# Kernel tuning notes

Measured on AMD Instinct MI355X. Metric: run time of the kernel, lower is better.

The kernel has to match this reference:

```python
import jax, jax.numpy as jnp
import numpy as np

N_NODES = 50000
N_EDGES = 800000
N_GRAPHS = 128
HIDDEN = 64
HEADS = 2
OUT = 4
NEG_SLOPE = 0.2
ALPHA_FLAG = 0.05


def _gat_conv(x, src, dst, W, a_src, a_dst, b):
    # PyG GATConv, concat=False (mean over heads), self-loops already appended.
    N = x.shape[0]
    H, C = a_src.shape
    xh = (x @ W).reshape(N, H, C)                       # [N,H,C]
    s_src = (xh * a_src).sum(-1)                        # [N,H]
    s_dst = (xh * a_dst).sum(-1)                        # [N,H]
    e = s_src[src] + s_dst[dst]                         # [E,H]
    e = jnp.where(e > 0, e, NEG_SLOPE * e)              # LeakyReLU(0.2)
    emax = jax.ops.segment_max(e, dst, num_segments=N)  # per-dst softmax max
    emax = jnp.where(jnp.isfinite(emax), emax, 0.0)
    p = jnp.exp(e - emax[dst])
    denom = jax.ops.segment_sum(p, dst, num_segments=N)
    alpha = p / (denom[dst] + 1e-16)                    # [E,H]
    out = jax.ops.segment_sum(alpha[:, :, None] * xh[src], dst, num_segments=N)
    return out.mean(axis=1) + b                         # [N,HIDDEN]


def setup_inputs() -> dict:
    key = jax.random.key(0)
    ks = jax.random.split(key, 32)
    f = lambda k, shape, s=0.1: (jax.random.normal(k, shape) * s).astype(jnp.float32)
    inp = {}
    inp['x_all'] = jax.random.normal(ks[0], (N_NODES, 8), dtype=jnp.float32)
    inp['climber'] = jax.random.normal(ks[1], (N_GRAPHS, 4), dtype=jnp.float32)
    inp['edge_index'] = jax.random.randint(ks[2], (2, N_EDGES), 0, N_NODES)
    inp['batch'] = jnp.sort(jax.random.randint(ks[3], (N_NODES,), 0, N_GRAPHS))
    H = HIDDEN
    inp['W_in'] = f(ks[4], (6, H)); inp['b_in'] = jnp.zeros((H,), jnp.float32)
    inp['W_c'] = f(ks[5], (4, H)); inp['b_c'] = jnp.zeros((H,), jnp.float32)
    inp['W_f1'] = f(ks[6], (H, 2 * H)); inp['b_f1'] = jnp.zeros((2 * H,), jnp.float32)
    inp['W_f2'] = f(ks[7], (H, 2 * H)); inp['b_f2'] = jnp.zeros((2 * H,), jnp.float32)
    inp['W_g1'] = f(ks[8], (H, HEADS * H)); inp['a_src1'] = f(ks[9], (HEADS, H)); inp['a_dst1'] = f(ks[10], (HEADS, H)); inp['b_g1'] = jnp.zeros((H,), jnp.float32)
    inp['W_g2'] = f(ks[11], (H, HEADS * H)); inp['a_src2'] = f(ks[12], (HEADS, H)); inp['a_dst2'] = f(ks[13], (HEADS, H)); inp['b_g2'] = jnp.zeros((H,), jnp.float32)
    inp['W_cl1'] = f(ks[14], (H, H)); inp['b_cl1'] = jnp.zeros((H,), jnp.float32)
    inp['W_cl2'] = f(ks[15], (H, OUT)); inp['b_cl2'] = jnp.zeros((OUT,), jnp.float32)
    inp['W_fh1'] = f(ks[16], (2, 8), 0.001); inp['b_fh1'] = jnp.zeros((8,), jnp.float32)
    inp['W_fh2'] = f(ks[17], (8, OUT), 0.001); inp['b_fh2'] = jnp.zeros((OUT,), jnp.float32)
    return inp


def reference(x_all, climber, edge_index, batch, W_in, b_in, W_c, b_c,
              W_f1, b_f1, W_f2, b_f2,
              W_g1, a_src1, a_dst1, b_g1,
              W_g2, a_src2, a_dst2, b_g2,
              W_cl1, b_cl1, W_cl2, b_cl2,
              W_fh1, b_fh1, W_fh2, b_fh2):
    N = x_all.shape[0]
    flags = x_all[:, -2:]
    x = x_all[:, :-2]
    # climber embedding (eval mode -> dropout is identity)
    c = jax.nn.relu(climber @ W_c + b_c)                 # [G,H]
    x = x @ W_in + b_in                                  # [N,H]
    # FiLM 1
    gb = c @ W_f1 + b_f1
    gamma, beta = jnp.split(gb, 2, axis=-1)
    x = x * (1.0 + gamma[batch]) + beta[batch]
    # add self-loops (PyG GATConv default)
    loop = jnp.arange(N, dtype=edge_index.dtype)
    src = jnp.concatenate([edge_index[0], loop])
    dst = jnp.concatenate([edge_index[1], loop])
    x = jax.nn.relu(_gat_conv(x, src, dst, W_g1, a_src1, a_dst1, b_g1))
    # FiLM 2
    gb = c @ W_f2 + b_f2
    gamma, beta = jnp.split(gb, 2, axis=-1)
    x = x * (1.0 + gamma[batch]) + beta[batch]
    x = jax.nn.relu(_gat_conv(x, src, dst, W_g2, a_src2, a_dst2, b_g2))
    logits_main = jax.nn.relu(x @ W_cl1 + b_cl1) @ W_cl2 + b_cl2
    logits_flag = jax.nn.relu(flags @ W_fh1 + b_fh1) @ W_fh2 + b_fh2
    return logits_main + ALPHA_FLAG * logits_flag
```

## Files before the change

kernel.cpp:

```cpp
#include <hip/hip_runtime.h>
#include <hip/hip_fp16.h>

#define NEG_SLOPE 0.2f
#define ALPHA_FLAG 0.05f

typedef _Float16 h2t __attribute__((ext_vector_type(2)));
union h2u { unsigned u; h2t h; __half2 hh; float f; };
static __device__ __forceinline__ h2t u_as_h2(unsigned u) { h2u c; c.u = u; return c.h; }
static __device__ __forceinline__ float h2_as_f(__half2 h) { h2u c; c.hh = h; return c.f; }
static __device__ __forceinline__ h2t f_as_h2(float f) { h2u c; c.f = f; return c.h; }

static inline size_t align256(size_t x) { return (x + 255) & ~(size_t)255; }

__global__ void prep_kernel(const float* __restrict__ climber,
                            const float* __restrict__ W_c, const float* __restrict__ b_c,
                            const float* __restrict__ W_f1, const float* __restrict__ b_f1,
                            const float* __restrict__ W_f2, const float* __restrict__ b_f2,
                            float* __restrict__ gb1, float* __restrict__ gb2) {
    __shared__ float c_sh[64];
    int g = blockIdx.x, t = threadIdx.x;
    if (t < 64) {
        float acc = b_c[t];
#pragma unroll
        for (int k = 0; k < 4; ++k) acc = fmaf(climber[g * 4 + k], W_c[k * 64 + t], acc);
        c_sh[t] = fmaxf(acc, 0.f);
    }
    __syncthreads();
    float a1 = b_f1[t], a2 = b_f2[t];
#pragma unroll 8
    for (int h = 0; h < 64; ++h) {
        float cv = c_sh[h];
        a1 = fmaf(cv, W_f1[h * 128 + t], a1);
        a2 = fmaf(cv, W_f2[h * 128 + t], a2);
    }
    gb1[g * 128 + t] = a1;
    gb2[g * 128 + t] = a2;
}

__global__ void init_counts_kernel(int* __restrict__ counts, int N) {
    int i = blockIdx.x * blockDim.x + threadIdx.x;
    if (i < N) counts[i] = 1;
}

__global__ void hist_kernel(const int* __restrict__ dst, int E, int* __restrict__ counts) {
    int i = blockIdx.x * blockDim.x + threadIdx.x;
    if (i < E) atomicAdd(&counts[dst[i]], 1);
}

#define SCAN_CHUNK 1024
__global__ void scan_partial_kernel(const int* __restrict__ counts, int* __restrict__ block_sums, int N) {
    __shared__ int sh[256];
    int b = blockIdx.x, t = threadIdx.x;
    int idx0 = b * SCAN_CHUNK + t * 4;
    int s = 0;
    if (idx0 + 3 < N) {
        int4 v = *(const int4*)&counts[idx0];
        s = v.x + v.y + v.z + v.w;
    } else {
#pragma unroll
        for (int u = 0; u < 4; ++u) if (idx0 + u < N) s += counts[idx0 + u];
    }
    sh[t] = s;
    __syncthreads();
#pragma unroll
    for (int off = 128; off; off >>= 1) {
        if (t < off) sh[t] += sh[t + off];
        __syncthreads();
    }
    if (t == 0) block_sums[b] = sh[0];
}

__global__ void scan_blocksums_kernel(const int* __restrict__ block_sums, int* __restrict__ block_bases,
                                      int nb, int* __restrict__ row_ptr, int N) {
    __shared__ int sh[256];
    int t = threadIdx.x;
    int v = (t < nb) ? block_sums[t] : 0;
    sh[t] = v;
    __syncthreads();
#pragma unroll
    for (int off = 1; off < 256; off <<= 1) {
        int add = (t >= off) ? sh[t - off] : 0;
        __syncthreads();
        sh[t] += add;
        __syncthreads();
    }
    if (t < nb) block_bases[t] = sh[t] - v;
    if (t == nb - 1) row_ptr[N] = sh[t];
}

__global__ void scan_final_kernel(const int* __restrict__ counts, const int* __restrict__ block_bases,
                                  int* __restrict__ row_ptr, int* __restrict__ fill, int N) {
    __shared__ int sh[256];
    int b = blockIdx.x, t = threadIdx.x;
    int idx0 = b * SCAN_CHUNK + t * 4;
    int c[4];
    if (idx0 + 3 < N) {
        int4 v = *(const int4*)&counts[idx0];
        c[0] = v.x; c[1] = v.y; c[2] = v.z; c[3] = v.w;
    } else {
#pragma unroll
        for (int u = 0; u < 4; ++u) c[u] = (idx0 + u < N) ? counts[idx0 + u] : 0;
    }
    int s = c[0] + c[1] + c[2] + c[3];
    sh[t] = s;
    __syncthreads();
#pragma unroll
    for (int off = 1; off < 256; off <<= 1) {
        int add = (t >= off) ? sh[t - off] : 0;
        __syncthreads();
        sh[t] += add;
        __syncthreads();
    }
    int run = block_bases[b] + sh[t] - s;
#pragma unroll
    for (int u = 0; u < 4; ++u) {
        if (idx0 + u < N) {
            row_ptr[idx0 + u] = run;
            fill[idx0 + u] = run;
            run += c[u];
        }
    }
}

__global__ void scatter_kernel(const int* __restrict__ src, const int* __restrict__ dst,
                               int E, int N, int* __restrict__ fill, int* __restrict__ csr_src) {
    int i = blockIdx.x * blockDim.x + threadIdx.x;
    if (i >= E + N) return;
    int s, d;
    if (i < E) { s = src[i]; d = dst[i]; }
    else       { s = i - E; d = s; }
    int pos = atomicAdd(&fill[d], 1);
    csr_src[pos] = s;
}

#define XH_NB 32
__global__ __launch_bounds__(256, 4) void xh_kernel(
    const float* __restrict__ x, const float* __restrict__ W_g,
    const float* __restrict__ a_src, const float* __restrict__ a_dst,
    __half* __restrict__ xh, float* __restrict__ s_src, float* __restrict__ s_dst,
    int N, int in_mode,
    const float* __restrict__ x_all, const int* __restrict__ batch,
    const float* __restrict__ W_in, const float* __restrict__ b_in,
    const float* __restrict__ gb1) {
    __shared__ float x_sh[XH_NB * 64];
    __shared__ float win_sh[6 * 64 + 64];
    int t = threadIdx.x;
    int base = blockIdx.x * XH_NB;
    if (in_mode) {
        for (int i = t; i < 448; i += 256)
            win_sh[i] = (i < 384) ? W_in[i] : b_in[i - 384];
        __syncthreads();
        int nd = t >> 3;
        int jb = (t & 7) * 8;
        int n = base + nd;
        if (n < N) {
            float4 a = *(const float4*)&x_all[(size_t)n * 8];
            float2 b = *(const float2*)&x_all[(size_t)n * 8 + 4];
            float xa[6] = {a.x, a.y, a.z, a.w, b.x, b.y};
            int g = batch[n];
            const float* gbrow = &gb1[g * 128];
#pragma unroll
            for (int jj = 0; jj < 8; ++jj) {
                int j = jb + jj;
                float acc = win_sh[384 + j];
#pragma unroll
                for (int k = 0; k < 6; ++k) acc = fmaf(xa[k], win_sh[k * 64 + j], acc);
                x_sh[nd * 64 + j] = acc * (1.f + gbrow[j]) + gbrow[64 + j];
            }
        } else {
#pragma unroll
            for (int jj = 0; jj < 8; ++jj) x_sh[nd * 64 + jb + jj] = 0.f;
        }
    } else {
        int nvalid = N - base; if (nvalid > XH_NB) nvalid = XH_NB;
        int nfloats = nvalid * 64;
#pragma unroll
        for (int rep = 0; rep < 2; ++rep) {
            int i = t * 4 + rep * 1024;
            float4 v = (i < nfloats) ? *(const float4*)&x[(size_t)base * 64 + i]
                                     : make_float4(0.f, 0.f, 0.f, 0.f);
            *(float4*)&x_sh[i] = v;
        }
    }
    __syncthreads();
    int c = t & 63;
    int g = t >> 6;
    float acc0[8], acc1[8];
#pragma unroll
    for (int i = 0; i < 8; ++i) { acc0[i] = 0.f; acc1[i] = 0.f; }
    const float* W0 = W_g + c;
    const float* W1 = W_g + 64 + c;
#pragma unroll 2
    for (int k = 0; k < 64; k += 4) {
        float w0[4], w1[4];
#pragma unroll
        for (int u = 0; u < 4; ++u) { w0[u] = W0[(k + u) * 128]; w1[u] = W1[(k + u) * 128]; }
#pragma unroll
        for (int i = 0; i < 8; ++i) {
            float4 xv = *(const float4*)&x_sh[(g * 8 + i) * 64 + k];
            acc0[i] = fmaf(xv.x, w0[0], acc0[i]);
            acc0[i] = fmaf(xv.y, w0[1], acc0[i]);
            acc0[i] = fmaf(xv.z, w0[2], acc0[i]);
            acc0[i] = fmaf(xv.w, w0[3], acc0[i]);
            acc1[i] = fmaf(xv.x, w1[0], acc1[i]);
            acc1[i] = fmaf(xv.y, w1[1], acc1[i]);
            acc1[i] = fmaf(xv.z, w1[2], acc1[i]);
            acc1[i] = fmaf(xv.w, w1[3], acc1[i]);
        }
    }
    float as0 = a_src[c], ad0 = a_dst[c];
    float as1 = a_src[64 + c], ad1 = a_dst[64 + c];
#pragma unroll
    for (int i = 0; i < 8; ++i) {
        int n = base + g * 8 + i;
        float ps0 = acc0[i] * as0, pd0 = acc0[i] * ad0;
        float ps1 = acc1[i] * as1, pd1 = acc1[i] * ad1;
#pragma unroll
        for (int off = 32; off; off >>= 1) {
            ps0 += __shfl_xor(ps0, off); pd0 += __shfl_xor(pd0, off);
            ps1 += __shfl_xor(ps1, off); pd1 += __shfl_xor(pd1, off);
        }
        if (n < N) {
            if (c == 0) {
                s_src[n * 2 + 0] = ps0; s_src[n * 2 + 1] = ps1;
                s_dst[n * 2 + 0] = pd0; s_dst[n * 2 + 1] = pd1;
            }
            __half2 hv = __floats2half2_rn(acc0[i], acc1[i]);
            *(__half2*)&xh[(size_t)n * 128 + c * 2] = hv;
        }
    }
}

static __device__ __forceinline__ float dot2acc(unsigned xbits, h2t w, float acc) {
#if __has_builtin(__builtin_amdgcn_fdot2)
    return __builtin_amdgcn_fdot2(u_as_h2(xbits), w, acc, false);
#else
    h2u cx; cx.u = xbits;
    float2 xf = __half22float2(cx.hh);
    h2u cw; cw.h = w;
    float2 wf = __half22float2(cw.hh);
    return fmaf(xf.x, wf.x, fmaf(xf.y, wf.y, acc));
#endif
}

__global__ __launch_bounds__(256) void agg_kernel(
    const __half* __restrict__ xh, const float* __restrict__ s_src,
    const float* __restrict__ s_dst, const int* __restrict__ row_ptr,
    const int* __restrict__ csr_src, const float* __restrict__ b_g,
    const int* __restrict__ batch, const float* __restrict__ gb_film,
    float* __restrict__ xout, int N, int mode,
    const float* __restrict__ x_all,
    const float* __restrict__ W_cl1, const float* __restrict__ b_cl1,
    const float* __restrict__ W_cl2, const float* __restrict__ b_cl2,
    const float* __restrict__ W_fh1, const float* __restrict__ b_fh1,
    const float* __restrict__ W_fh2, const float* __restrict__ b_fh2,
    float* __restrict__ out) {
    __shared__ float2 ps_sh[4][64];
    __shared__ float vh_sh[4][64];
    int lane = threadIdx.x & 63;
    int w = threadIdx.x >> 6;
    int n = (blockIdx.x * blockDim.x + threadIdx.x) >> 6;
    if (n >= N) return;
    int beg = row_ptr[n], end = row_ptr[n + 1];
    int deg = end - beg;
    float2 sd = *(const float2*)&s_dst[n * 2];
    const char* xhb = (const char*)xh;
    int sub = lane >> 4;
    unsigned q16 = (unsigned)(lane & 15) * 16u;
    float acc[4] = {0.f, 0.f, 0.f, 0.f};

    if (deg <= 64) {
        float p0 = 0.f, p1 = 0.f; unsigned sb = 0;
        if (lane < deg) {
            int s = csr_src[beg + lane];
            sb = (unsigned)s << 8;
            float2 ss = *(const float2*)&s_src[s * 2];
            float e0 = ss.x + sd.x, e1 = ss.y + sd.y;
            e0 = (e0 > 0.f) ? e0 : NEG_SLOPE * e0;
            e1 = (e1 > 0.f) ? e1 : NEG_SLOPE * e1;
            p0 = __expf(e0); p1 = __expf(e1);
        }
        float dp0 = p0, dp1 = p1;
#pragma unroll
        for (int off = 32; off; off >>= 1) {
            dp0 += __shfl_xor(dp0, off);
            dp1 += __shfl_xor(dp1, off);
        }
        float i0 = 0.5f / (dp0 + 1e-16f), i1 = 0.5f / (dp1 + 1e-16f);
        ps_sh[w][lane] = make_float2(h2_as_f(__floats2half2_rn(p0 * i0, p1 * i1)),
                                     __uint_as_float(sb));
        int mr = (deg + 3) & ~3;
        for (int j = 0; j < mr; j += 4) {
            float2 ps = ps_sh[w][j + sub];
            h2t wpk = f_as_h2(ps.x);
            unsigned voff = __float_as_uint(ps.y) + q16;
            uint4 hv = *(const uint4*)(xhb + voff);
            acc[0] = dot2acc(hv.x, wpk, acc[0]);
            acc[1] = dot2acc(hv.y, wpk, acc[1]);
            acc[2] = dot2acc(hv.z, wpk, acc[2]);
            acc[3] = dot2acc(hv.w, wpk, acc[3]);
        }
    } else {
        float dp0 = 0.f, dp1 = 0.f;
        for (int chunk = beg; chunk < end; chunk += 64) {
            int m = end - chunk; if (m > 64) m = 64;
            if (lane < m) {
                int s = csr_src[chunk + lane];
                float2 ss = *(const float2*)&s_src[s * 2];
                float e0 = ss.x + sd.x, e1 = ss.y + sd.y;
                e0 = (e0 > 0.f) ? e0 : NEG_SLOPE * e0;
                e1 = (e1 > 0.f) ? e1 : NEG_SLOPE * e1;
                dp0 += __expf(e0); dp1 += __expf(e1);
            }
        }
#pragma unroll
        for (int off = 32; off; off >>= 1) {
            dp0 += __shfl_xor(dp0, off);
            dp1 += __shfl_xor(dp1, off);
        }
        float i0 = 0.5f / (dp0 + 1e-16f), i1 = 0.5f / (dp1 + 1e-16f);
        for (int chunk = beg; chunk < end; chunk += 64) {
            int m = end - chunk; if (m > 64) m = 64;
            float p0 = 0.f, p1 = 0.f; unsigned sb = 0;
            if (lane < m) {
                int s = csr_src[chunk + lane];
                sb = (unsigned)s << 8;
                float2 ss = *(const float2*)&s_src[s * 2];
                float e0 = ss.x + sd.x, e1 = ss.y + sd.y;
                e0 = (e0 > 0.f) ? e0 : NEG_SLOPE * e0;
                e1 = (e1 > 0.f) ? e1 : NEG_SLOPE * e1;
                p0 = __expf(e0); p1 = __expf(e1);
            }
            ps_sh[w][lane] = make_float2(h2_as_f(__floats2half2_rn(p0 * i0, p1 * i1)),
                                         __uint_as_float(sb));
            int mr = (m + 3) & ~3;
            for (int j = 0; j < mr; j += 4) {
                float2 ps = ps_sh[w][j + sub];
                h2t wpk = f_as_h2(ps.x);
                unsigned voff = __float_as_uint(ps.y) + q16;
                uint4 hv = *(const uint4*)(xhb + voff);
                acc[0] = dot2acc(hv.x, wpk, acc[0]);
                acc[1] = dot2acc(hv.y, wpk, acc[1]);
                acc[2] = dot2acc(hv.z, wpk, acc[2]);
                acc[3] = dot2acc(hv.w, wpk, acc[3]);
            }
        }
    }
#pragma unroll
    for (int u = 0; u < 4; ++u) {
        acc[u] += __shfl_xor(acc[u], 16);
        acc[u] += __shfl_xor(acc[u], 32);
    }
    if (lane < 16) *(float4*)&vh_sh[w][lane * 4] = make_float4(acc[0], acc[1], acc[2], acc[3]);
    float v = vh_sh[w][lane] + b_g[lane];
    v = fmaxf(v, 0.f);
    if (mode == 0) {
        int g = batch[n];
        v = v * (1.f + gb_film[g * 128 + lane]) + gb_film[g * 128 + 64 + lane];
        xout[(size_t)n * 64 + lane] = v;
        return;
    }
    vh_sh[w][lane] = v;
    float h = b_cl1[lane];
#pragma unroll 4
    for (int k = 0; k < 64; k += 4) {
        float4 vq = *(const float4*)&vh_sh[w][k];
        h = fmaf(vq.x, W_cl1[(k + 0) * 64 + lane], h);
        h = fmaf(vq.y, W_cl1[(k + 1) * 64 + lane], h);
        h = fmaf(vq.z, W_cl1[(k + 2) * 64 + lane], h);
        h = fmaf(vq.w, W_cl1[(k + 3) * 64 + lane], h);
    }
    h = fmaxf(h, 0.f);
    float4 w2 = *(const float4*)&W_cl2[lane * 4];
    float o0 = h * w2.x, o1 = h * w2.y, o2 = h * w2.z, o3 = h * w2.w;
#pragma unroll
    for (int off = 32; off; off >>= 1) {
        o0 += __shfl_xor(o0, off); o1 += __shfl_xor(o1, off);
        o2 += __shfl_xor(o2, off); o3 += __shfl_xor(o3, off);
    }
    if (lane < 4) {
        float f0 = x_all[(size_t)n * 8 + 6], f1 = x_all[(size_t)n * 8 + 7];
        float lf = b_fh2[lane];
#pragma unroll
        for (int m = 0; m < 8; ++m) {
            float fm = fmaxf(fmaf(f0, W_fh1[m], fmaf(f1, W_fh1[8 + m], b_fh1[m])), 0.f);
            lf = fmaf(fm, W_fh2[m * 4 + lane], lf);
        }
        float om = (lane == 0) ? o0 : (lane == 1) ? o1 : (lane == 2) ? o2 : o3;
        out[(size_t)n * 4 + lane] = om + b_cl2[lane] + ALPHA_FLAG * lf;
    }
}

extern "C" void kernel_launch(void* const* d_in, const int* in_sizes, int n_in,
                              void* d_out, int out_size, void* d_ws, size_t ws_size,
                              hipStream_t stream) {
    const float* x_all   = (const float*)d_in[0];
    const float* climber = (const float*)d_in[1];
    const int*   eidx    = (const int*)d_in[2];
    const int*   batch   = (const int*)d_in[3];
    const float* W_in  = (const float*)d_in[4];
    const float* b_in  = (const float*)d_in[5];
    const float* W_c   = (const float*)d_in[6];
    const float* b_c   = (const float*)d_in[7];
    const float* W_f1  = (const float*)d_in[8];
    const float* b_f1  = (const float*)d_in[9];
    const float* W_f2  = (const float*)d_in[10];
    const float* b_f2  = (const float*)d_in[11];
    const float* W_g1  = (const float*)d_in[12];
    const float* a_s1  = (const float*)d_in[13];
    const float* a_d1  = (const float*)d_in[14];
    const float* b_g1  = (const float*)d_in[15];
    const float* W_g2  = (const float*)d_in[16];
    const float* a_s2  = (const float*)d_in[17];
    const float* a_d2  = (const float*)d_in[18];
    const float* b_g2  = (const float*)d_in[19];
    const float* W_cl1 = (const float*)d_in[20];
    const float* b_cl1 = (const float*)d_in[21];
    const float* W_cl2 = (const float*)d_in[22];
    const float* b_cl2 = (const float*)d_in[23];
    const float* W_fh1 = (const float*)d_in[24];
    const float* b_fh1 = (const float*)d_in[25];
    const float* W_fh2 = (const float*)d_in[26];
    const float* b_fh2 = (const float*)d_in[27];
    float* out = (float*)d_out;

    const int N = in_sizes[0] / 8;
    const int E = in_sizes[2] / 2;
    const int G = in_sizes[1] / 4;
    const int* src = eidx;
    const int* dst = eidx + E;
    const int NB_SCAN = (N + SCAN_CHUNK - 1) / SCAN_CHUNK;

    char* ws = (char*)d_ws;
    size_t off = 0;
    auto alloc = [&](size_t bytes) { char* p = ws + off; off += align256(bytes); return p; };
    float*  gb1     = (float*)alloc((size_t)G * 128 * 4);
    float*  gb2     = (float*)alloc((size_t)G * 128 * 4);
    float*  xbuf    = (float*)alloc((size_t)N * 64 * 4);
    __half* xh      = (__half*)alloc((size_t)N * 128 * 2);
    float*  s_src   = (float*)alloc((size_t)N * 2 * 4);
    float*  s_dst   = (float*)alloc((size_t)N * 2 * 4);
    int*    counts  = (int*)alloc((size_t)N * 4);
    int*    fill    = (int*)alloc((size_t)N * 4);
    int*    row_ptr = (int*)alloc((size_t)(N + 1) * 4);
    int*    csr_src = (int*)alloc((size_t)(E + N) * 4);
    int*    bsums   = (int*)alloc((size_t)256 * 4);
    int*    bbases  = (int*)alloc((size_t)256 * 4);
    (void)ws_size;

    prep_kernel<<<G, 128, 0, stream>>>(climber, W_c, b_c, W_f1, b_f1, W_f2, b_f2, gb1, gb2);
    init_counts_kernel<<<(N + 255) / 256, 256, 0, stream>>>(counts, N);
    hist_kernel<<<(E + 255) / 256, 256, 0, stream>>>(dst, E, counts);
    scan_partial_kernel<<<NB_SCAN, 256, 0, stream>>>(counts, bsums, N);
    scan_blocksums_kernel<<<1, 256, 0, stream>>>(bsums, bbases, NB_SCAN, row_ptr, N);
    scan_final_kernel<<<NB_SCAN, 256, 0, stream>>>(counts, bbases, row_ptr, fill, N);
    scatter_kernel<<<(E + N + 255) / 256, 256, 0, stream>>>(src, dst, E, N, fill, csr_src);
    xh_kernel<<<(N + XH_NB - 1) / XH_NB, 256, 0, stream>>>(nullptr, W_g1, a_s1, a_d1, xh,
                                                           s_src, s_dst, N, 1,
                                                           x_all, batch, W_in, b_in, gb1);
    agg_kernel<<<(N * 64 + 255) / 256, 256, 0, stream>>>(xh, s_src, s_dst, row_ptr, csr_src,
                                                         b_g1, batch, gb2, xbuf, N, 0,
                                                         nullptr, nullptr, nullptr, nullptr,
                                                         nullptr, nullptr, nullptr, nullptr,
                                                         nullptr, nullptr);
    xh_kernel<<<(N + XH_NB - 1) / XH_NB, 256, 0, stream>>>(xbuf, W_g2, a_s2, a_d2, xh,
                                                           s_src, s_dst, N, 0,
                                                           nullptr, nullptr, nullptr, nullptr, nullptr);
    agg_kernel<<<(N * 64 + 255) / 256, 256, 0, stream>>>(xh, s_src, s_dst, row_ptr, csr_src,
                                                         b_g2, batch, nullptr, nullptr, N, 1,
                                                         x_all, W_cl1, b_cl1, W_cl2, b_cl2,
                                                         W_fh1, b_fh1, W_fh2, b_fh2, out);
}
```

Baseline: 266.0 us.

## Trim CSR-build launches, vectorize atomics, store intermediate features in fp16

Replaces the count-init kernel with a memset and folds the self-loop +1 into the scan. The block-sum scan kernel is merged into the final scan through a per-block wavefront reduction. The histogram and scatter kernels now process 4 or 2 edges per thread with vector loads. The layer-1 output buffer is stored as fp16, halving its write and read traffic. The aggregation kernel is split into templated specialisations per mode. The aim is fewer kernel launches and less memory traffic, at the cost of extra rounding on the intermediate features.

```diff
diff --git a/kernel.cpp b/kernel.cpp
--- a/kernel.cpp
+++ b/kernel.cpp
@@ -37,14 +37,18 @@
     gb2[g * 128 + t] = a2;
 }
 
-__global__ void init_counts_kernel(int* __restrict__ counts, int N) {
-    int i = blockIdx.x * blockDim.x + threadIdx.x;
-    if (i < N) counts[i] = 1;
-}
-
 __global__ void hist_kernel(const int* __restrict__ dst, int E, int* __restrict__ counts) {
-    int i = blockIdx.x * blockDim.x + threadIdx.x;
-    if (i < E) atomicAdd(&counts[dst[i]], 1);
+    int i4 = (blockIdx.x * blockDim.x + threadIdx.x) * 4;
+    if (i4 + 3 < E) {
+        int4 d = *(const int4*)&dst[i4];
+        atomicAdd(&counts[d.x], 1);
+        atomicAdd(&counts[d.y], 1);
+        atomicAdd(&counts[d.z], 1);
+        atomicAdd(&counts[d.w], 1);
+    } else {
+        for (int u = 0; u < 4; ++u)
+            if (i4 + u < E) atomicAdd(&counts[dst[i4 + u]], 1);
+    }
 }
 
 #define SCAN_CHUNK 1024
@@ -55,10 +59,10 @@
     int s = 0;
     if (idx0 + 3 < N) {
         int4 v = *(const int4*)&counts[idx0];
-        s = v.x + v.y + v.z + v.w;
-    } else {
-#pragma unroll
-        for (int u = 0; u < 4; ++u) if (idx0 + u < N) s += counts[idx0 + u];
+        s = v.x + v.y + v.z + v.w + 4;
+    } else {
+#pragma unroll
+        for (int u = 0; u < 4; ++u) if (idx0 + u < N) s += counts[idx0 + u] + 1;
     }
     sh[t] = s;
     __syncthreads();
@@ -70,12 +74,28 @@
     if (t == 0) block_sums[b] = sh[0];
 }
 
-__global__ void scan_blocksums_kernel(const int* __restrict__ block_sums, int* __restrict__ block_bases,
-                                      int nb, int* __restrict__ row_ptr, int N) {
+__global__ void scan_final_kernel(const int* __restrict__ counts, const int* __restrict__ block_sums,
+                                  int nb, int* __restrict__ row_ptr, int* __restrict__ fill, int N) {
     __shared__ int sh[256];
-    int t = threadIdx.x;
-    int v = (t < nb) ? block_sums[t] : 0;
-    sh[t] = v;
+    __shared__ int base_sh;
+    int b = blockIdx.x, t = threadIdx.x;
+    if (t < 64) {
+        int v = (t < nb && t < b) ? block_sums[t] : 0;
+#pragma unroll
+        for (int off = 32; off; off >>= 1) v += __shfl_xor(v, off);
+        if (t == 0) base_sh = v;
+    }
+    int idx0 = b * SCAN_CHUNK + t * 4;
+    int c[4];
+    if (idx0 + 3 < N) {
+        int4 v = *(const int4*)&counts[idx0];
+        c[0] = v.x + 1; c[1] = v.y + 1; c[2] = v.z + 1; c[3] = v.w + 1;
+    } else {
+#pragma unroll
+        for (int u = 0; u < 4; ++u) c[u] = (idx0 + u < N) ? counts[idx0 + u] + 1 : 0;
+    }
+    int s = c[0] + c[1] + c[2] + c[3];
+    sh[t] = s;
     __syncthreads();
 #pragma unroll
     for (int off = 1; off < 256; off <<= 1) {
@@ -84,58 +104,35 @@
         sh[t] += add;
         __syncthreads();
     }
-    if (t < nb) block_bases[t] = sh[t] - v;
-    if (t == nb - 1) row_ptr[N] = sh[t];
-}
-
-__global__ void scan_final_kernel(const int* __restrict__ counts, const int* __restrict__ block_bases,
-                                  int* __restrict__ row_ptr, int* __restrict__ fill, int N) {
-    __shared__ int sh[256];
-    int b = blockIdx.x, t = threadIdx.x;
-    int idx0 = b * SCAN_CHUNK + t * 4;
-    int c[4];
-    if (idx0 + 3 < N) {
-        int4 v = *(const int4*)&counts[idx0];
-        c[0] = v.x; c[1] = v.y; c[2] = v.z; c[3] = v.w;
-    } else {
-#pragma unroll
-        for (int u = 0; u < 4; ++u) c[u] = (idx0 + u < N) ? counts[idx0 + u] : 0;
-    }
-    int s = c[0] + c[1] + c[2] + c[3];
-    sh[t] = s;
-    __syncthreads();
-#pragma unroll
-    for (int off = 1; off < 256; off <<= 1) {
-        int add = (t >= off) ? sh[t - off] : 0;
-        __syncthreads();
-        sh[t] += add;
-        __syncthreads();
-    }
-    int run = block_bases[b] + sh[t] - s;
+    int run = base_sh + sh[t] - s;
 #pragma unroll
     for (int u = 0; u < 4; ++u) {
         if (idx0 + u < N) {
             row_ptr[idx0 + u] = run;
             fill[idx0 + u] = run;
             run += c[u];
+            if (idx0 + u == N - 1) row_ptr[N] = run;
         }
     }
 }
 
 __global__ void scatter_kernel(const int* __restrict__ src, const int* __restrict__ dst,
-                               int E, int N, int* __restrict__ fill, int* __restrict__ csr_src) {
-    int i = blockIdx.x * blockDim.x + threadIdx.x;
-    if (i >= E + N) return;
-    int s, d;
-    if (i < E) { s = src[i]; d = dst[i]; }
-    else       { s = i - E; d = s; }
-    int pos = atomicAdd(&fill[d], 1);
-    csr_src[pos] = s;
+                               int Eh, int N, int* __restrict__ fill, int* __restrict__ csr_src) {
+    int t = blockIdx.x * blockDim.x + threadIdx.x;
+    if (t < Eh) {
+        int2 s2 = *(const int2*)&src[t * 2];
+        int2 d2 = *(const int2*)&dst[t * 2];
+        int p0 = atomicAdd(&fill[d2.x], 1); csr_src[p0] = s2.x;
+        int p1 = atomicAdd(&fill[d2.y], 1); csr_src[p1] = s2.y;
+    } else {
+        int i = t - Eh;
+        if (i < N) { int p = atomicAdd(&fill[i], 1); csr_src[p] = i; }
+    }
 }
 
 #define XH_NB 32
 __global__ __launch_bounds__(256, 4) void xh_kernel(
-    const float* __restrict__ x, const float* __restrict__ W_g,
+    const __half* __restrict__ xhalf, const float* __restrict__ W_g,
     const float* __restrict__ a_src, const float* __restrict__ a_dst,
     __half* __restrict__ xh, float* __restrict__ s_src, float* __restrict__ s_dst,
     int N, int in_mode,
@@ -173,14 +170,18 @@
         }
     } else {
         int nvalid = N - base; if (nvalid > XH_NB) nvalid = XH_NB;
-        int nfloats = nvalid * 64;
-#pragma unroll
-        for (int rep = 0; rep < 2; ++rep) {
-            int i = t * 4 + rep * 1024;
-            float4 v = (i < nfloats) ? *(const float4*)&x[(size_t)base * 64 + i]
-                                     : make_float4(0.f, 0.f, 0.f, 0.f);
-            *(float4*)&x_sh[i] = v;
-        }
+        int nhalves = nvalid * 64;
+        int idx = t * 8;
+        uint4 raw = make_uint4(0, 0, 0, 0);
+        if (idx < nhalves) raw = *(const uint4*)&xhalf[(size_t)base * 64 + idx];
+        float2 f0 = __half22float2(*(__half2*)&raw.x);
+        float2 f1 = __half22float2(*(__half2*)&raw.y);
+        float2 f2 = __half22float2(*(__half2*)&raw.z);
+        float2 f3 = __half22float2(*(__half2*)&raw.w);
+        x_sh[idx + 0] = f0.x; x_sh[idx + 1] = f0.y;
+        x_sh[idx + 2] = f1.x; x_sh[idx + 3] = f1.y;
+        x_sh[idx + 4] = f2.x; x_sh[idx + 5] = f2.y;
+        x_sh[idx + 6] = f3.x; x_sh[idx + 7] = f3.y;
     }
     __syncthreads();
     int c = t & 63;
@@ -243,12 +244,13 @@
 #endif
 }
 
-__global__ __launch_bounds__(256) void agg_kernel(
+template <int MODE>
+static __device__ __forceinline__ void agg_impl(
     const __half* __restrict__ xh, const float* __restrict__ s_src,
     const float* __restrict__ s_dst, const int* __restrict__ row_ptr,
     const int* __restrict__ csr_src, const float* __restrict__ b_g,
     const int* __restrict__ batch, const float* __restrict__ gb_film,
-    float* __restrict__ xout, int N, int mode,
+    __half* __restrict__ xout_h, int N,
     const float* __restrict__ x_all,
     const float* __restrict__ W_cl1, const float* __restrict__ b_cl1,
     const float* __restrict__ W_cl2, const float* __restrict__ b_cl2,
@@ -354,10 +356,10 @@
     if (lane < 16) *(float4*)&vh_sh[w][lane * 4] = make_float4(acc[0], acc[1], acc[2], acc[3]);
     float v = vh_sh[w][lane] + b_g[lane];
     v = fmaxf(v, 0.f);
-    if (mode == 0) {
+    if (MODE == 0) {
         int g = batch[n];
         v = v * (1.f + gb_film[g * 128 + lane]) + gb_film[g * 128 + 64 + lane];
-        xout[(size_t)n * 64 + lane] = v;
+        xout_h[(size_t)n * 64 + lane] = __float2half(v);
         return;
     }
     vh_sh[w][lane] = v;
@@ -389,6 +391,25 @@
         float om = (lane == 0) ? o0 : (lane == 1) ? o1 : (lane == 2) ? o2 : o3;
         out[(size_t)n * 4 + lane] = om + b_cl2[lane] + ALPHA_FLAG * lf;
     }
+}
+
+__global__ __launch_bounds__(256) void agg_film_kernel(
+    const __half* xh, const float* s_src, const float* s_dst, const int* row_ptr,
+    const int* csr_src, const float* b_g, const int* batch, const float* gb_film,
+    __half* xout_h, int N) {
+    agg_impl<0>(xh, s_src, s_dst, row_ptr, csr_src, b_g, batch, gb_film, xout_h, N,
+                nullptr, nullptr, nullptr, nullptr, nullptr, nullptr, nullptr,
+                nullptr, nullptr, nullptr);
+}
+
+__global__ __launch_bounds__(256) void agg_cls_kernel(
+    const __half* xh, const float* s_src, const float* s_dst, const int* row_ptr,
+    const int* csr_src, const float* b_g, int N, const float* x_all,
+    const float* W_cl1, const float* b_cl1, const float* W_cl2, const float* b_cl2,
+    const float* W_fh1, const float* b_fh1, const float* W_fh2, const float* b_fh2,
+    float* out) {
+    agg_impl<1>(xh, s_src, s_dst, row_ptr, csr_src, b_g, nullptr, nullptr, nullptr, N,
+                x_all, W_cl1, b_cl1, W_cl2, b_cl2, W_fh1, b_fh1, W_fh2, b_fh2, out);
 }
 
 extern "C" void kernel_launch(void* const* d_in, const int* in_sizes, int n_in,
@@ -436,7 +457,7 @@
     auto alloc = [&](size_t bytes) { char* p = ws + off; off += align256(bytes); return p; };
     float*  gb1     = (float*)alloc((size_t)G * 128 * 4);
     float*  gb2     = (float*)alloc((size_t)G * 128 * 4);
-    float*  xbuf    = (float*)alloc((size_t)N * 64 * 4);
+    __half* xbuf    = (__half*)alloc((size_t)N * 64 * 2);
     __half* xh      = (__half*)alloc((size_t)N * 128 * 2);
     float*  s_src   = (float*)alloc((size_t)N * 2 * 4);
     float*  s_dst   = (float*)alloc((size_t)N * 2 * 4);
@@ -444,30 +465,25 @@
     int*    fill    = (int*)alloc((size_t)N * 4);
     int*    row_ptr = (int*)alloc((size_t)(N + 1) * 4);
     int*    csr_src = (int*)alloc((size_t)(E + N) * 4);
-    int*    bsums   = (int*)alloc((size_t)256 * 4);
-    int*    bbases  = (int*)alloc((size_t)256 * 4);
+    int*    bsums   = (int*)alloc((size_t)64 * 4);
     (void)ws_size;
 
     prep_kernel<<<G, 128, 0, stream>>>(climber, W_c, b_c, W_f1, b_f1, W_f2, b_f2, gb1, gb2);
-    init_counts_kernel<<<(N + 255) / 256, 256, 0, stream>>>(counts, N);
-    hist_kernel<<<(E + 255) / 256, 256, 0, stream>>>(dst, E, counts);
+    hipMemsetAsync(counts, 0, (size_t)N * 4, stream);
+    hist_kernel<<<(E / 4 + 255) / 256, 256, 0, stream>>>(dst, E, counts);
     scan_partial_kernel<<<NB_SCAN, 256, 0, stream>>>(counts, bsums, N);
-    scan_blocksums_kernel<<<1, 256, 0, stream>>>(bsums, bbases, NB_SCAN, row_ptr, N);
-    scan_final_kernel<<<NB_SCAN, 256, 0, stream>>>(counts, bbases, row_ptr, fill, N);
-    scatter_kernel<<<(E + N + 255) / 256, 256, 0, stream>>>(src, dst, E, N, fill, csr_src);
+    scan_final_kernel<<<NB_SCAN, 256, 0, stream>>>(counts, bsums, NB_SCAN, row_ptr, fill, N);
+    scatter_kernel<<<(E / 2 + N + 255) / 256, 256, 0, stream>>>(src, dst, E / 2, N, fill, csr_src);
     xh_kernel<<<(N + XH_NB - 1) / XH_NB, 256, 0, stream>>>(nullptr, W_g1, a_s1, a_d1, xh,
                                                            s_src, s_dst, N, 1,
                                                            x_all, batch, W_in, b_in, gb1);
-    agg_kernel<<<(N * 64 + 255) / 256, 256, 0, stream>>>(xh, s_src, s_dst, row_ptr, csr_src,
-                                                         b_g1, batch, gb2, xbuf, N, 0,
-                                                         nullptr, nullptr, nullptr, nullptr,
-                                                         nullptr, nullptr, nullptr, nullptr,
-                                                         nullptr, nullptr);
+    agg_film_kernel<<<(N * 64 + 255) / 256, 256, 0, stream>>>(xh, s_src, s_dst, row_ptr, csr_src,
+                                                              b_g1, batch, gb2, xbuf, N);
     xh_kernel<<<(N + XH_NB - 1) / XH_NB, 256, 0, stream>>>(xbuf, W_g2, a_s2, a_d2, xh,
                                                            s_src, s_dst, N, 0,
                                                            nullptr, nullptr, nullptr, nullptr, nullptr);
-    agg_kernel<<<(N * 64 + 255) / 256, 256, 0, stream>>>(xh, s_src, s_dst, row_ptr, csr_src,
-                                                         b_g2, batch, nullptr, nullptr, N, 1,
-                                                         x_all, W_cl1, b_cl1, W_cl2, b_cl2,
-                                                         W_fh1, b_fh1, W_fh2, b_fh2, out);
-}
+    agg_cls_kernel<<<(N * 64 + 255) / 256, 256, 0, stream>>>(xh, s_src, s_dst, row_ptr, csr_src,
+                                                             b_g2, N, x_all, W_cl1, b_cl1,
+                                                             W_cl2, b_cl2, W_fh1, b_fh1,
+                                                             W_fh2, b_fh2, out);
+}
```

After: 257.5 us. 1.03x faster.
